# Optimization experiments

Hardware: AMD Instinct MI355X
Metric: run time of the kernel (lower is better)

The kernel has to match this reference:

```python
import jax, jax.numpy as jnp
import numpy as np

N_TRAIN = 131072
M_TEST = 65536
T_SPAN = 100.0
D = 3  # Matern-5/2 state dim


def setup_inputs() -> dict:
    key = jax.random.key(0)
    k1, k2, k3, k4 = jax.random.split(key, 4)
    times = jnp.sort(jax.random.uniform(k1, (N_TRAIN,), jnp.float32) * T_SPAN)
    t_star = jnp.sort(jax.random.uniform(k2, (M_TEST,), jnp.float32) * T_SPAN)
    # positive site precisions, site naturals scaled so pseudo-targets are O(1)
    site_nat2 = jax.random.uniform(k3, (N_TRAIN,), jnp.float32) * 4.0 + 0.5
    site_nat1 = jax.random.normal(k4, (N_TRAIN,), jnp.float32) * site_nat2
    return dict(
        times=times,
        t_star=t_star,
        site_nat1=site_nat1,
        site_nat2=site_nat2,
        variance=jnp.float32(1.0),
        lengthscale=jnp.float32(0.5),
        mean_const=jnp.float32(0.1),
    )


def _matern52_sde(variance, lengthscale):
    lam = jnp.sqrt(5.0).astype(jnp.float32) / lengthscale
    F = jnp.array([[0.0, 1.0, 0.0],
                   [0.0, 0.0, 1.0],
                   [0.0, 0.0, 0.0]], jnp.float32)
    F = F.at[2, 0].set(-lam ** 3).at[2, 1].set(-3.0 * lam ** 2).at[2, 2].set(-3.0 * lam)
    kappa = lam ** 2 / 3.0
    P_inf = variance * jnp.array([[1.0, 0.0, 0.0],
                                  [0.0, 0.0, 0.0],
                                  [0.0, 0.0, 0.0]], jnp.float32)
    P_inf = P_inf.at[0, 2].set(-variance * kappa)
    P_inf = P_inf.at[2, 0].set(-variance * kappa)
    P_inf = P_inf.at[1, 1].set(variance * kappa)
    P_inf = P_inf.at[2, 2].set(variance * lam ** 4)
    H = jnp.array([[1.0, 0.0, 0.0]], jnp.float32)
    return F, H, P_inf, lam


def _discretise(F, P_inf, lam, dt):
    # (F + lam I) is nilpotent of index 3 -> exact expm
    I = jnp.eye(D, dtype=jnp.float32)
    Nm = F + lam * I
    Nm2 = Nm @ Nm
    dt_ = dt[:, None, None]
    A = jnp.exp(-lam * dt)[:, None, None] * (I + dt_ * Nm + 0.5 * dt_ ** 2 * Nm2)
    APA = jnp.einsum('tij,jk,tlk->til', A, P_inf, A)
    Q = P_inf - APA
    return A, Q


def _kalman_filter(H, P_inf, A_seq, Q_seq, residual, is_obs, R_full):
    h = H[0]  # [D]

    def step(carry, inp):
        m, P = carry
        A, Q, r, obs, R = inp
        m_pred = A @ m
        P_pred = A @ P @ A.T + Q
        S = h @ P_pred @ h + R
        K = obs * (P_pred @ h) / S  # masked gain: test points skip update
        v = r - m_pred @ h
        m_f = m_pred + K * v
        P_f = P_pred - jnp.outer(K, K) * S
        return (m_f, P_f), (m_pred, P_pred, m_f, P_f)

    init = (jnp.zeros(D, jnp.float32), P_inf)
    _, (m_pred, P_pred, m_filt, P_filt) = jax.lax.scan(
        step, init, (A_seq, Q_seq, residual, is_obs, R_full))
    return m_pred, P_pred, m_filt, P_filt


def _rts_smoother(m_pred, P_pred, m_filt, P_filt, A_seq):
    def back(carry, inp):
        m_s_next, P_s_next = carry
        m_f, P_f, A_n, m_p_n, P_p_n = inp
        G = jnp.linalg.solve(P_p_n, A_n @ P_f).T  # P_f A^T P_pred^{-1}
        m_s = m_f + G @ (m_s_next - m_p_n)
        P_s = P_f + G @ (P_s_next - P_p_n) @ G.T
        return (m_s, P_s), (m_s, P_s)

    init = (m_filt[-1], P_filt[-1])
    xs = (m_filt[:-1], P_filt[:-1], A_seq[1:], m_pred[1:], P_pred[1:])
    _, (m_s, P_s) = jax.lax.scan(back, init, xs, reverse=True)
    m_smooth = jnp.concatenate([m_s, m_filt[-1:]], axis=0)
    P_smooth = jnp.concatenate([P_s, P_filt[-1:]], axis=0)
    return m_smooth, P_smooth


def reference(times, t_star, site_nat1, site_nat2, variance, lengthscale, mean_const):
    F, H, P_inf, lam = _matern52_sde(variance, lengthscale)
    N = times.shape[0]
    M = t_star.shape[0]
    merged = jnp.concatenate([times, t_star])
    order = jnp.argsort(merged)  # jnp.argsort is stable
    merged_sorted = merged[order]
    is_obs = jnp.concatenate([jnp.ones(N, jnp.float32), jnp.zeros(M, jnp.float32)])[order]
    pseudo_targets = site_nat1 / site_nat2
    residual_full = jnp.concatenate([pseudo_targets - mean_const,
                                     jnp.zeros(M, jnp.float32)])[order]
    R_full = jnp.concatenate([jnp.reciprocal(site_nat2), jnp.ones(M, jnp.float32)])[order]
    dt_full = jnp.concatenate([jnp.zeros(1, jnp.float32), jnp.diff(merged_sorted)])
    A_seq, Q_seq = _discretise(F, P_inf, lam, dt_full)
    m_pred, P_pred, m_filt, P_filt = _kalman_filter(
        H, P_inf, A_seq, Q_seq, residual_full, is_obs, R_full)
    m_smooth, P_smooth = _rts_smoother(m_pred, P_pred, m_filt, P_filt, A_seq)
    inv_order = jnp.argsort(order)
    test_positions = inv_order[N:]
    m_test = m_smooth[test_positions]
    P_test = P_smooth[test_positions]
    means = m_test @ H[0] + mean_const  # H = [1,0,0]
    vars_ = jnp.einsum('i,tij,j->t', H[0], P_test, H[0])
    return means, jnp.maximum(vars_, 0.0)
```

## Files before the change

kernel.cpp:

```cpp
#include <hip/hip_runtime.h>
#include <math.h>

#define DEV __device__ __forceinline__

constexpr int N_TRAIN = 131072;
constexpr int M_TEST  = 65536;
constexpr int T_TOT   = N_TRAIN + M_TEST;
constexpr int TPB     = 64;
constexpr int NBLK    = T_TOT / TPB;
constexpr int GRP     = 64;
constexpr int NGRP    = NBLK / GRP;
constexpr int FE_P    = 27;

DEV void mm(const float* X, const float* Y, float* Z) {
#pragma unroll
  for (int i = 0; i < 3; ++i)
#pragma unroll
    for (int j = 0; j < 3; ++j)
      Z[i*3+j] = X[i*3]*Y[j] + X[i*3+1]*Y[3+j] + X[i*3+2]*Y[6+j];
}
DEV void mmnt(const float* X, const float* Y, float* Z) {
#pragma unroll
  for (int i = 0; i < 3; ++i)
#pragma unroll
    for (int j = 0; j < 3; ++j)
      Z[i*3+j] = X[i*3]*Y[j*3] + X[i*3+1]*Y[j*3+1] + X[i*3+2]*Y[j*3+2];
}
DEV void mtn(const float* X, const float* Y, float* Z) {
#pragma unroll
  for (int i = 0; i < 3; ++i)
#pragma unroll
    for (int j = 0; j < 3; ++j)
      Z[i*3+j] = X[i]*Y[j] + X[3+i]*Y[3+j] + X[6+i]*Y[6+j];
}
DEV void mv(const float* X, const float* v, float* w) {
#pragma unroll
  for (int i = 0; i < 3; ++i) w[i] = X[i*3]*v[0] + X[i*3+1]*v[1] + X[i*3+2]*v[2];
}
DEV void mtv(const float* X, const float* v, float* w) {
#pragma unroll
  for (int i = 0; i < 3; ++i) w[i] = X[i]*v[0] + X[3+i]*v[1] + X[6+i]*v[2];
}
DEV void inv3f(const float* m, float* o) {
  float c00 = m[4]*m[8] - m[5]*m[7];
  float c10 = m[5]*m[6] - m[3]*m[8];
  float c20 = m[3]*m[7] - m[4]*m[6];
  float det = m[0]*c00 + m[1]*c10 + m[2]*c20;
  float id = 1.0f / det;
  o[0] = c00*id; o[1] = (m[2]*m[7]-m[1]*m[8])*id; o[2] = (m[1]*m[5]-m[2]*m[4])*id;
  o[3] = c10*id; o[4] = (m[0]*m[8]-m[2]*m[6])*id; o[5] = (m[2]*m[3]-m[0]*m[5])*id;
  o[6] = c20*id; o[7] = (m[1]*m[6]-m[0]*m[7])*id; o[8] = (m[0]*m[4]-m[1]*m[3])*id;
}
DEV void inv3d(const float* mf_, float* o) {
  double m0=mf_[0], m1=mf_[1], m2=mf_[2], m3=mf_[3], m4=mf_[4],
         m5=mf_[5], m6=mf_[6], m7=mf_[7], m8=mf_[8];
  double c00 = m4*m8 - m5*m7;
  double c10 = m5*m6 - m3*m8;
  double c20 = m3*m7 - m4*m6;
  double det = m0*c00 + m1*c10 + m2*c20;
  double id = 1.0 / det;
  o[0] = (float)(c00*id); o[1] = (float)((m2*m7-m1*m8)*id); o[2] = (float)((m1*m5-m2*m4)*id);
  o[3] = (float)(c10*id); o[4] = (float)((m0*m8-m2*m6)*id); o[5] = (float)((m2*m3-m0*m5)*id);
  o[6] = (float)(c20*id); o[7] = (float)((m1*m6-m0*m7)*id); o[8] = (float)((m0*m4-m1*m3)*id);
}
DEV void symm(float* P) {
  float a = 0.5f*(P[1]+P[3]), b = 0.5f*(P[2]+P[6]), c = 0.5f*(P[5]+P[7]);
  P[1]=P[3]=a; P[2]=P[6]=b; P[5]=P[7]=c;
}
DEV void st_state(const float* m, const float* P, float* g) {
  g[0]=m[0]; g[1]=m[1]; g[2]=m[2];
  g[3]=P[0]; g[4]=P[1]; g[5]=P[2]; g[6]=P[4]; g[7]=P[5]; g[8]=P[8];
}
DEV void ld_state(const float* g, float* m, float* P) {
  m[0]=g[0]; m[1]=g[1]; m[2]=g[2];
  P[0]=g[3]; P[1]=g[4]; P[2]=g[5];
  P[3]=g[4]; P[4]=g[6]; P[5]=g[7];
  P[6]=g[5]; P[7]=g[7]; P[8]=g[8];
}

struct Model { float lam, v, kap, l4; };
DEV Model make_model(const float* varp, const float* ellp) {
  Model M; M.v = varp[0];
  float ell = ellp[0];
  M.lam = sqrtf(5.0f) / ell;
  M.kap = M.lam * M.lam / 3.0f;
  float l2 = M.lam * M.lam;
  M.l4 = l2 * l2;
  return M;
}
DEV void pinf(const Model& M, float* P) {
  float vk = M.v * M.kap;
  P[0]=M.v; P[1]=0;  P[2]=-vk;
  P[3]=0;   P[4]=vk; P[5]=0;
  P[6]=-vk; P[7]=0;  P[8]=M.v*M.l4;
}
DEV void make_AQ(const Model& M, float dt, float* A, float* Q) {
  float lam = M.lam, l2 = lam*lam, l3 = l2*lam, l4 = M.l4;
  float e = __expf(-lam * dt);
  float h = 0.5f * dt * dt;
  A[0] = e*(1.0f + dt*lam + h*l2);
  A[1] = e*(dt + 2.0f*h*lam);
  A[2] = e*h;
  A[3] = e*(-h*l3);
  A[4] = e*(1.0f + dt*lam - 2.0f*h*l2);
  A[5] = e*(dt - h*lam);
  A[6] = e*(-dt*l3 + h*l4);
  A[7] = e*(-3.0f*dt*l2 + 2.0f*h*l3);
  A[8] = e*(1.0f - 2.0f*dt*lam + h*l2);
  float vk = M.v * M.kap, vl4 = M.v * M.l4;
  float B[9];
#pragma unroll
  for (int i = 0; i < 3; ++i) {
    B[i*3+0] =  A[i*3+0]*M.v - A[i*3+2]*vk;
    B[i*3+1] =  A[i*3+1]*vk;
    B[i*3+2] = -A[i*3+0]*vk  + A[i*3+2]*vl4;
  }
  float Pi[9]; pinf(M, Pi);
#pragma unroll
  for (int i = 0; i < 3; ++i)
#pragma unroll
    for (int j = 0; j < 3; ++j)
      Q[i*3+j] = Pi[i*3+j] - (B[i*3]*A[j*3] + B[i*3+1]*A[j*3+1] + B[i*3+2]*A[j*3+2]);
}

struct FE { float A[9]; float b[3]; float C[9]; float h[3]; float J[9]; };

DEV FE fe_identity() {
  FE e;
#pragma unroll
  for (int i=0;i<9;++i){ e.A[i]=0.0f; e.C[i]=0.0f; e.J[i]=0.0f; }
  e.A[0]=e.A[4]=e.A[8]=1.0f;
  e.b[0]=e.b[1]=e.b[2]=0.0f; e.h[0]=e.h[1]=e.h[2]=0.0f;
  return e;
}
DEV void fe_store27(const FE& e, float* g) {
#pragma unroll
  for (int i=0;i<9;++i) g[i]=e.A[i];
  g[9]=e.b[0]; g[10]=e.b[1]; g[11]=e.b[2];
  g[12]=e.C[0]; g[13]=e.C[1]; g[14]=e.C[2]; g[15]=e.C[4]; g[16]=e.C[5]; g[17]=e.C[8];
  g[18]=e.h[0]; g[19]=e.h[1]; g[20]=e.h[2];
  g[21]=e.J[0]; g[22]=e.J[1]; g[23]=e.J[2]; g[24]=e.J[4]; g[25]=e.J[5]; g[26]=e.J[8];
}
DEV FE fe_load27(const float* g) {
  FE e;
#pragma unroll
  for (int i=0;i<9;++i) e.A[i]=g[i];
  e.b[0]=g[9]; e.b[1]=g[10]; e.b[2]=g[11];
  e.C[0]=g[12]; e.C[1]=g[13]; e.C[2]=g[14]; e.C[3]=g[13]; e.C[4]=g[15];
  e.C[5]=g[16]; e.C[6]=g[14]; e.C[7]=g[16]; e.C[8]=g[17];
  e.h[0]=g[18]; e.h[1]=g[19]; e.h[2]=g[20];
  e.J[0]=g[21]; e.J[1]=g[22]; e.J[2]=g[23]; e.J[3]=g[22]; e.J[4]=g[24];
  e.J[5]=g[25]; e.J[6]=g[23]; e.J[7]=g[25]; e.J[8]=g[26];
  return e;
}
DEV void fe_storeT(const FE& e, float* g, int idx, int n) {
#pragma unroll
  for (int i=0;i<9;++i) g[i*n+idx]=e.A[i];
#pragma unroll
  for (int i=0;i<3;++i) g[(9+i)*n+idx]=e.b[i];
  g[12*n+idx]=e.C[0]; g[13*n+idx]=e.C[1]; g[14*n+idx]=e.C[2];
  g[15*n+idx]=e.C[4]; g[16*n+idx]=e.C[5]; g[17*n+idx]=e.C[8];
#pragma unroll
  for (int i=0;i<3;++i) g[(18+i)*n+idx]=e.h[i];
  g[21*n+idx]=e.J[0]; g[22*n+idx]=e.J[1]; g[23*n+idx]=e.J[2];
  g[24*n+idx]=e.J[4]; g[25*n+idx]=e.J[5]; g[26*n+idx]=e.J[8];
}
DEV FE fe_loadT(const float* g, int idx, int n) {
  FE e;
#pragma unroll
  for (int i=0;i<9;++i) e.A[i]=g[i*n+idx];
#pragma unroll
  for (int i=0;i<3;++i) e.b[i]=g[(9+i)*n+idx];
  float c0=g[12*n+idx], c1=g[13*n+idx], c2=g[14*n+idx],
        c4=g[15*n+idx], c5=g[16*n+idx], c8=g[17*n+idx];
  e.C[0]=c0; e.C[1]=c1; e.C[2]=c2; e.C[3]=c1; e.C[4]=c4; e.C[5]=c5;
  e.C[6]=c2; e.C[7]=c5; e.C[8]=c8;
#pragma unroll
  for (int i=0;i<3;++i) e.h[i]=g[(18+i)*n+idx];
  float j0=g[21*n+idx], j1=g[22*n+idx], j2=g[23*n+idx],
        j4=g[24*n+idx], j5=g[25*n+idx], j8=g[26*n+idx];
  e.J[0]=j0; e.J[1]=j1; e.J[2]=j2; e.J[3]=j1; e.J[4]=j4; e.J[5]=j5;
  e.J[6]=j2; e.J[7]=j5; e.J[8]=j8;
  return e;
}
DEV void fe_loadT_state(const float* g, int idx, int n, float* m, float* P) {
#pragma unroll
  for (int i=0;i<3;++i) m[i]=g[(9+i)*n+idx];
  float c0=g[12*n+idx], c1=g[13*n+idx], c2=g[14*n+idx],
        c4=g[15*n+idx], c5=g[16*n+idx], c8=g[17*n+idx];
  P[0]=c0; P[1]=c1; P[2]=c2; P[3]=c1; P[4]=c4; P[5]=c5; P[6]=c2; P[7]=c5; P[8]=c8;
}
DEV FE fe_shfl_up(const FE& e, int d) {
  FE o;
#pragma unroll
  for (int i=0;i<9;++i) o.A[i]=__shfl_up(e.A[i], d, 64);
#pragma unroll
  for (int i=0;i<3;++i) o.b[i]=__shfl_up(e.b[i], d, 64);
  float c0=__shfl_up(e.C[0],d,64), c1=__shfl_up(e.C[1],d,64), c2=__shfl_up(e.C[2],d,64),
        c4=__shfl_up(e.C[4],d,64), c5=__shfl_up(e.C[5],d,64), c8=__shfl_up(e.C[8],d,64);
  o.C[0]=c0; o.C[1]=c1; o.C[2]=c2; o.C[3]=c1; o.C[4]=c4; o.C[5]=c5;
  o.C[6]=c2; o.C[7]=c5; o.C[8]=c8;
#pragma unroll
  for (int i=0;i<3;++i) o.h[i]=__shfl_up(e.h[i], d, 64);
  float j0=__shfl_up(e.J[0],d,64), j1=__shfl_up(e.J[1],d,64), j2=__shfl_up(e.J[2],d,64),
        j4=__shfl_up(e.J[4],d,64), j5=__shfl_up(e.J[5],d,64), j8=__shfl_up(e.J[8],d,64);
  o.J[0]=j0; o.J[1]=j1; o.J[2]=j2; o.J[3]=j1; o.J[4]=j4; o.J[5]=j5;
  o.J[6]=j2; o.J[7]=j5; o.J[8]=j8;
  return o;
}
DEV FE build_felem(const Model& M, float dt, float obsf, float rf, float Rf_, bool first) {
  FE E;
  float r = rf, R = Rf_;
  float g = (obsf > 0.5f) ? 1.0f : 0.0f;
  if (first) {
#pragma unroll
    for (int i=0;i<9;++i){ E.A[i]=0.0f; E.J[i]=0.0f; }
    E.h[0]=E.h[1]=E.h[2]=0.0f;
    float Pi[9]; pinf(M, Pi);
    float S = Pi[0] + R;
    float f = g / S;
    float K0=Pi[0]*f, K1=Pi[3]*f, K2=Pi[6]*f;
    E.b[0]=K0*r; E.b[1]=K1*r; E.b[2]=K2*r;
    E.C[0]=Pi[0]-S*K0*K0; E.C[1]=Pi[1]-S*K0*K1; E.C[2]=Pi[2]-S*K0*K2;
    E.C[3]=Pi[3]-S*K1*K0; E.C[4]=Pi[4]-S*K1*K1; E.C[5]=Pi[5]-S*K1*K2;
    E.C[6]=Pi[6]-S*K2*K0; E.C[7]=Pi[7]-S*K2*K1; E.C[8]=Pi[8]-S*K2*K2;
    return E;
  }
  float Am[9], Q[9]; make_AQ(M, dt, Am, Q);
  float S = Q[0] + R, iS = g / S;
  float K0=Q[0]*iS, K1=Q[3]*iS, K2=Q[6]*iS;
#pragma unroll
  for (int j = 0; j < 3; ++j) {
    E.A[j]   = Am[j]   - K0*Am[j];
    E.A[3+j] = Am[3+j] - K1*Am[j];
    E.A[6+j] = Am[6+j] - K2*Am[j];
    E.C[j]   = Q[j]    - K0*Q[j];
    E.C[3+j] = Q[3+j]  - K1*Q[j];
    E.C[6+j] = Q[6+j]  - K2*Q[j];
  }
  E.b[0]=K0*r; E.b[1]=K1*r; E.b[2]=K2*r;
  float riS = r*iS;
  E.h[0]=Am[0]*riS; E.h[1]=Am[1]*riS; E.h[2]=Am[2]*riS;
#pragma unroll
  for (int i = 0; i < 3; ++i)
#pragma unroll
    for (int j = 0; j < 3; ++j)
      E.J[i*3+j] = Am[i]*Am[j]*iS;
  return E;
}
DEV FE fcompose(const FE& x, const FE& y) {
  const float *A1=x.A,*b1=x.b,*C1=x.C,*h1=x.h,*J1=x.J;
  const float *A2=y.A,*b2=y.b,*C2=y.C,*h2=y.h,*J2=y.J;
  FE o;
  float Mx[9]; mm(C1,J2,Mx); Mx[0]+=1.0f; Mx[4]+=1.0f; Mx[8]+=1.0f;
  float Mi[9]; inv3f(Mx,Mi);
  float T1[9]; mm(A2,Mi,T1);
  mm(T1,A1,o.A);
  float u[3]; mv(C1,h2,u); u[0]+=b1[0]; u[1]+=b1[1]; u[2]+=b1[2];
  mv(T1,u,o.b); o.b[0]+=b2[0]; o.b[1]+=b2[1]; o.b[2]+=b2[2];
  float t2[9]; mm(T1,C1,t2);
  mmnt(t2,A2,o.C);
#pragma unroll
  for (int i=0;i<9;++i) o.C[i]+=C2[i];
  float tmp[9]; mm(Mi,A1,tmp);
  float w[3]; mv(J2,b1,w);
  w[0]=h2[0]-w[0]; w[1]=h2[1]-w[1]; w[2]=h2[2]-w[2];
  mtv(tmp,w,o.h); o.h[0]+=h1[0]; o.h[1]+=h1[1]; o.h[2]+=h1[2];
  float V[9]; mm(J2,A1,V);
  mtn(tmp,V,o.J);
#pragma unroll
  for (int i=0;i<9;++i) o.J[i]+=J1[i];
  symm(o.C); symm(o.J);
  return o;
}
DEV void fapply(const FE& y, float* m, float* P) {
  float Mx[9]; mm(P, y.J, Mx); Mx[0]+=1.0f; Mx[4]+=1.0f; Mx[8]+=1.0f;
  float Mi[9]; inv3f(Mx, Mi);
  float T1[9]; mm(y.A, Mi, T1);
  float u[3]; mv(P, y.h, u); u[0]+=m[0]; u[1]+=m[1]; u[2]+=m[2];
  float mn[3]; mv(T1, u, mn);
  m[0]=mn[0]+y.b[0]; m[1]=mn[1]+y.b[1]; m[2]=mn[2]+y.b[2];
  float t2[9]; mm(T1, P, t2);
  float Pn[9]; mmnt(t2, y.A, Pn);
#pragma unroll
  for (int i=0;i<9;++i) P[i]=Pn[i]+y.C[i];
  symm(P);
}
DEV void fstep(const Model& M, float dt, float obsf, float rf, float Rf_,
               float* m, float* P) {
  float A[9], Q[9]; make_AQ(M, dt, A, Q);
  float mp[3]; mv(A, m, mp);
  float W[9]; mmnt(P, A, W);
  float Pp[9]; mm(A, W, Pp);
#pragma unroll
  for (int i=0;i<9;++i) Pp[i]+=Q[i];
  float S = Pp[0] + Rf_;
  float f = (obsf > 0.5f) ? (1.0f/S) : 0.0f;
  float K0=Pp[0]*f, K1=Pp[3]*f, K2=Pp[6]*f;
  float v = rf - mp[0];
  m[0]=mp[0]+K0*v; m[1]=mp[1]+K1*v; m[2]=mp[2]+K2*v;
  P[0]=Pp[0]-S*K0*K0; P[1]=Pp[1]-S*K0*K1; P[2]=Pp[2]-S*K0*K2;
  P[3]=Pp[3]-S*K1*K0; P[4]=Pp[4]-S*K1*K1; P[5]=Pp[5]-S*K1*K2;
  P[6]=Pp[6]-S*K2*K0; P[7]=Pp[7]-S*K2*K1; P[8]=Pp[8]-S*K2*K2;
  symm(P);
}

struct SE { float G[9]; float c[3]; float U[9]; };

DEV SE se_identity() {
  SE s;
#pragma unroll
  for (int i=0;i<9;++i){ s.G[i]=0.0f; s.U[i]=0.0f; }
  s.G[0]=s.G[4]=s.G[8]=1.0f;
  s.c[0]=s.c[1]=s.c[2]=0.0f;
  return s;
}
DEV void se_store(const SE& s, float* g) {
#pragma unroll
  for (int i=0;i<9;++i) g[i]=s.G[i];
  g[9]=s.c[0]; g[10]=s.c[1]; g[11]=s.c[2];
  g[12]=s.U[0]; g[13]=s.U[1]; g[14]=s.U[2]; g[15]=s.U[4]; g[16]=s.U[5]; g[17]=s.U[8];
}
DEV SE se_load(const float* g) {
  SE s;
#pragma unroll
  for (int i=0;i<9;++i) s.G[i]=g[i];
  s.c[0]=g[9]; s.c[1]=g[10]; s.c[2]=g[11];
  s.U[0]=g[12]; s.U[1]=g[13]; s.U[2]=g[14];
  s.U[3]=g[13]; s.U[4]=g[15]; s.U[5]=g[16];
  s.U[6]=g[14]; s.U[7]=g[16]; s.U[8]=g[17];
  return s;
}
DEV void se_storeT(const SE& s, float* g, int idx, int n) {
#pragma unroll
  for (int i=0;i<9;++i) g[i*n+idx]=s.G[i];
#pragma unroll
  for (int i=0;i<3;++i) g[(9+i)*n+idx]=s.c[i];
  g[12*n+idx]=s.U[0]; g[13*n+idx]=s.U[1]; g[14*n+idx]=s.U[2];
  g[15*n+idx]=s.U[4]; g[16*n+idx]=s.U[5]; g[17*n+idx]=s.U[8];
}
DEV SE se_loadT(const float* g, int idx, int n) {
  SE s;
#pragma unroll
  for (int i=0;i<9;++i) s.G[i]=g[i*n+idx];
#pragma unroll
  for (int i=0;i<3;++i) s.c[i]=g[(9+i)*n+idx];
  float u0=g[12*n+idx], u1=g[13*n+idx], u2=g[14*n+idx],
        u4=g[15*n+idx], u5=g[16*n+idx], u8=g[17*n+idx];
  s.U[0]=u0; s.U[1]=u1; s.U[2]=u2;
  s.U[3]=u1; s.U[4]=u4; s.U[5]=u5;
  s.U[6]=u2; s.U[7]=u5; s.U[8]=u8;
  return s;
}
DEV SE se_shfl_down(const SE& s, int d) {
  SE o;
#pragma unroll
  for (int i=0;i<9;++i) o.G[i]=__shfl_down(s.G[i], d, 64);
#pragma unroll
  for (int i=0;i<3;++i) o.c[i]=__shfl_down(s.c[i], d, 64);
  float u0=__shfl_down(s.U[0],d,64), u1=__shfl_down(s.U[1],d,64), u2=__shfl_down(s.U[2],d,64),
        u4=__shfl_down(s.U[4],d,64), u5=__shfl_down(s.U[5],d,64), u8=__shfl_down(s.U[8],d,64);
  o.U[0]=u0; o.U[1]=u1; o.U[2]=u2; o.U[3]=u1; o.U[4]=u4; o.U[5]=u5;
  o.U[6]=u2; o.U[7]=u5; o.U[8]=u8;
  return o;
}
DEV SE scompose(const SE& x, const SE& y) {
  SE o;
  mm(x.G, y.G, o.G);
  float t[3]; mv(x.G, y.c, t);
  o.c[0]=t[0]+x.c[0]; o.c[1]=t[1]+x.c[1]; o.c[2]=t[2]+x.c[2];
  float T[9]; mm(x.G, y.U, T);
  mmnt(T, x.G, o.U);
#pragma unroll
  for (int i=0;i<9;++i) o.U[i]+=x.U[i];
  symm(o.U);
  return o;
}
DEV void sapply(const SE& s, float* m, float* P) {
  float t[3]; mv(s.G, m, t);
  float T[9]; mm(s.G, P, T);
  float Pn[9]; mmnt(T, s.G, Pn);
  m[0]=t[0]+s.c[0]; m[1]=t[1]+s.c[1]; m[2]=t[2]+s.c[2];
#pragma unroll
  for (int i=0;i<9;++i) P[i]=Pn[i]+s.U[i];
  symm(P);
}
DEV SE selem_from_state(const Model& M, const float* m, const float* P, float dtn) {
  SE s;
  float A[9], Q[9]; make_AQ(M, dtn, A, Q);
  float W[9]; mmnt(P, A, W);
  float Pp[9]; mm(A, W, Pp);
#pragma unroll
  for (int j=0;j<9;++j) Pp[j]+=Q[j];
  float Pi_[9]; inv3d(Pp, Pi_);
  mm(W, Pi_, s.G);
  float mp[3]; mv(A, m, mp);
  float gm[3]; mv(s.G, mp, gm);
  s.c[0]=m[0]-gm[0]; s.c[1]=m[1]-gm[1]; s.c[2]=m[2]-gm[2];
  float GW[9]; mmnt(s.G, W, GW);
#pragma unroll
  for (int j=0;j<9;++j) s.U[j]=P[j]-GW[j];
  symm(s.U);
  return s;
}

__global__ void k_merge(const float* __restrict__ times, const float* __restrict__ tstar,
                        const float* __restrict__ n1, const float* __restrict__ n2,
                        const float* __restrict__ mcp,
                        float4* pk, int* oix) {
  int g = blockIdx.x*blockDim.x + threadIdx.x;
  if (g >= T_TOT) return;
  float mc = mcp[0];
  if (g < N_TRAIN) {
    int i = g;
    float t = times[i];
    int lo = 0, hi = M_TEST;
    while (lo < hi) { int mid=(lo+hi)>>1; if (tstar[mid] < t) lo=mid+1; else hi=mid; }
    int p = i + lo;
    float s2 = n2[i];
    pk[p] = make_float4(t, n1[i]/s2 - mc, 1.0f/s2, 1.0f);
    oix[p] = -1;
  } else {
    int j = g - N_TRAIN;
    float t = tstar[j];
    int lo = 0, hi = N_TRAIN;
    while (lo < hi) { int mid=(lo+hi)>>1; if (times[mid] <= t) lo=mid+1; else hi=mid; }
    int p = j + lo;
    pk[p] = make_float4(t, 0.f, 1.f, 0.f);
    oix[p] = j;
  }
}

__global__ __launch_bounds__(TPB) void k_f1(
    const float* varp, const float* ellp, const float4* __restrict__ pk,
    float* tIncl, float* blkAgg) {
  int l = threadIdx.x, b = blockIdx.x;
  int t = b*TPB + l;
  Model M = make_model(varp, ellp);
  float4 q = pk[t];
  float dt = (t == 0) ? 0.0f : (q.x - pk[t-1].x);
  FE run = build_felem(M, dt, q.w, q.y, q.z, t == 0);
  for (int d = 1; d < TPB; d <<= 1) {
    FE oth = fe_shfl_up(run, d);
    FE comp = fcompose(oth, run);
    if (l >= d) run = comp;
  }
  fe_storeT(run, tIncl, t, T_TOT);
  if (l == TPB-1) fe_storeT(run, blkAgg, b, NBLK);
}

__global__ __launch_bounds__(TPB) void k_f2a(const float* __restrict__ blkAgg,
                                             float* blkIncl2, float* grpAgg) {
  int l = threadIdx.x, gb = blockIdx.x;
  int b = gb*GRP + l;
  FE run = fe_loadT(blkAgg, b, NBLK);
  for (int d = 1; d < TPB; d <<= 1) {
    FE oth = fe_shfl_up(run, d);
    FE comp = fcompose(oth, run);
    if (l >= d) run = comp;
  }
  fe_storeT(run, blkIncl2, b, NBLK);
  if (l == GRP-1) fe_store27(run, grpAgg + gb*FE_P);
}

__global__ __launch_bounds__(TPB) void k_f2b(const float* __restrict__ grpAgg,
                                             float* grpPref) {
  int j = threadIdx.x;
  FE run = (j < NGRP) ? fe_load27(grpAgg + j*FE_P) : fe_identity();
  for (int d = 1; d < TPB; d <<= 1) {
    FE oth = fe_shfl_up(run, d);
    FE comp = fcompose(oth, run);
    if (j >= d) run = comp;
  }
  FE X = fe_shfl_up(run, 1);
  if (j < NGRP) {
    if (j == 0) X = fe_identity();
    fe_store27(X, grpPref + j*FE_P);
  }
}

__global__ __launch_bounds__(TPB) void k_f3(
    const float* varp, const float* ellp, const float4* __restrict__ pk,
    const float* __restrict__ tIncl, const float* __restrict__ blkIncl2,
    const float* __restrict__ grpPref,
    float* out5, float* blkAggS, float* xT) {
  int l = threadIdx.x, b = blockIdx.x;
  int t = b*TPB + l;
  int g = b >> 6, lb = b & (GRP-1);
  Model M = make_model(varp, ellp);
  float m[3], P[9];
  if (t == 0) {
    m[0]=m[1]=m[2]=0.0f; pinf(M, P);
  } else if (g == 0 && lb == 0) {
    fe_loadT_state(tIncl, t-1, T_TOT, m, P);
  } else if (g == 0) {
    fe_loadT_state(blkIncl2, b-1, NBLK, m, P);
    if (l > 0) { FE y = fe_loadT(tIncl, t-1, T_TOT); fapply(y, m, P); }
  } else {
    const float* gp = grpPref + g*FE_P;
    m[0]=gp[9]; m[1]=gp[10]; m[2]=gp[11];
    P[0]=gp[12]; P[1]=gp[13]; P[2]=gp[14];
    P[3]=gp[13]; P[4]=gp[15]; P[5]=gp[16];
    P[6]=gp[14]; P[7]=gp[16]; P[8]=gp[17];
    if (lb > 0) { FE y = fe_loadT(blkIncl2, b-1, NBLK); fapply(y, m, P); }
    if (l  > 0) { FE y = fe_loadT(tIncl,  t-1, T_TOT); fapply(y, m, P); }
  }
  float4 q = pk[t];
  float dt = (t == 0) ? 0.0f : (q.x - pk[t-1].x);
  fstep(M, dt, q.w, q.y, q.z, m, P);
  SE e;
  if (t < T_TOT-1) {
    float dtn = pk[t+1].x - q.x;
    e = selem_from_state(M, m, P, dtn);
  } else {
    e = se_identity();
    xT[0]=m[0]; xT[1]=m[1]; xT[2]=m[2];
    xT[3]=P[0]; xT[4]=P[1]; xT[5]=P[2];
    xT[6]=P[4]; xT[7]=P[5]; xT[8]=P[8];
  }
  SE Macc = e;
  for (int d = 1; d < TPB; d <<= 1) {
    SE oth = se_shfl_down(Macc, d);
    SE c = scompose(Macc, oth);
    if (l + d < TPB) Macc = c;
  }
  out5[0*T_TOT+t] = Macc.G[0];
  out5[1*T_TOT+t] = Macc.G[1];
  out5[2*T_TOT+t] = Macc.G[2];
  out5[3*T_TOT+t] = Macc.c[0];
  out5[4*T_TOT+t] = Macc.U[0];
  if (l == 0) se_storeT(Macc, blkAggS, b, NBLK);
}

__global__ __launch_bounds__(TPB) void k_s2a(const float* __restrict__ blkAggS,
                                             float* blkSuf2, float* grpAggS) {
  int l = threadIdx.x, gb = blockIdx.x;
  int b = gb*GRP + l;
  SE run = se_loadT(blkAggS, b, NBLK);
  for (int d = 1; d < TPB; d <<= 1) {
    SE oth = se_shfl_down(run, d);
    SE comp = scompose(run, oth);
    if (l + d < TPB) run = comp;
  }
  se_storeT(run, blkSuf2, b, NBLK);
  if (l == 0) se_store(run, grpAggS + gb*18);
}

__global__ __launch_bounds__(TPB) void k_s2b(const float* __restrict__ grpAggS,
                                             const float* __restrict__ xT,
                                             float* gExit) {
  int j = threadIdx.x;
  SE run = (j < NGRP) ? se_load(grpAggS + j*18) : se_identity();
  for (int d = 1; d < TPB; d <<= 1) {
    SE oth = se_shfl_down(run, d);
    SE comp = scompose(run, oth);
    if (j + d < TPB) run = comp;
  }
  SE Sx = se_shfl_down(run, 1);
  if (j < NGRP) {
    float m[3] = { xT[0], xT[1], xT[2] };
    float P[9] = { xT[3],xT[4],xT[5], xT[4],xT[6],xT[7], xT[5],xT[7],xT[8] };
    if (j < NGRP-1) sapply(Sx, m, P);
    st_state(m, P, gExit + j*9);
  }
}

__global__ __launch_bounds__(256) void k_s3(
    const float* mcp, const float* __restrict__ out5,
    const float* __restrict__ blkSuf2, const float* __restrict__ gExit,
    const int* __restrict__ oix, float* out) {
  int t = blockIdx.x*256 + threadIdx.x;
  int b = t >> 6;
  int g = b >> 6, lb = b & (GRP-1);
  float mc = mcp[0];
  float m[3], P[9];
  ld_state(gExit + g*9, m, P);
  if (lb < GRP-1) {
    SE s = se_loadT(blkSuf2, b+1, NBLK);
    sapply(s, m, P);
  }
  float g0 = out5[0*T_TOT+t], g1 = out5[1*T_TOT+t], g2 = out5[2*T_TOT+t];
  float c0 = out5[3*T_TOT+t], u00 = out5[4*T_TOT+t];
  float mm0 = g0*m[0] + g1*m[1] + g2*m[2] + c0;
  float q0 = g0*P[0] + g1*P[3] + g2*P[6];
  float q1 = g0*P[1] + g1*P[4] + g2*P[7];
  float q2 = g0*P[2] + g1*P[5] + g2*P[8];
  float v00 = q0*g0 + q1*g1 + q2*g2 + u00;
  int j = oix[t];
  if (j >= 0) { out[j] = mm0 + mc; out[M_TEST + j] = fmaxf(v00, 0.0f); }
}

extern "C" void kernel_launch(void* const* d_in, const int* in_sizes, int n_in,
                              void* d_out, int out_size, void* d_ws, size_t ws_size,
                              hipStream_t stream) {
  const float* times = (const float*)d_in[0];
  const float* tstar = (const float*)d_in[1];
  const float* n1    = (const float*)d_in[2];
  const float* n2    = (const float*)d_in[3];
  const float* varp  = (const float*)d_in[4];
  const float* ellp  = (const float*)d_in[5];
  const float* mcp   = (const float*)d_in[6];
  float* out = (float*)d_out;

  size_t off = 0;
  auto take = [&](size_t bytes) {
    char* p = (char*)d_ws + off;
    off += (bytes + 255) & ~(size_t)255;
    return (void*)p;
  };
  float4* pk     = (float4*)take(sizeof(float4) * T_TOT);
  int*    oix    = (int*)   take(sizeof(int)    * T_TOT);
  float*  tIncl  = (float*) take(sizeof(float)  * FE_P * T_TOT);
  float*  blkAgg = (float*) take(sizeof(float)  * FE_P * NBLK);
  float*  blkIncl2=(float*) take(sizeof(float)  * FE_P * NBLK);
  float*  grpAgg = (float*) take(sizeof(float)  * FE_P * NGRP);
  float*  grpPref= (float*) take(sizeof(float)  * FE_P * NGRP);
  float*  out5   = (float*) take(sizeof(float)  * 5  * T_TOT);
  float*  blkAggS= (float*) take(sizeof(float)  * 18 * NBLK);
  float*  blkSuf2= (float*) take(sizeof(float)  * 18 * NBLK);
  float*  grpAggS= (float*) take(sizeof(float)  * 18 * NGRP);
  float*  gExit  = (float*) take(sizeof(float)  * 9  * NGRP);
  float*  xT     = (float*) take(sizeof(float)  * 9);
  (void)ws_size; (void)in_sizes; (void)n_in; (void)out_size;

  k_merge<<<(T_TOT+255)/256, 256, 0, stream>>>(times, tstar, n1, n2, mcp, pk, oix);
  k_f1   <<<NBLK, TPB, 0, stream>>>(varp, ellp, pk, tIncl, blkAgg);
  k_f2a  <<<NGRP, TPB, 0, stream>>>(blkAgg, blkIncl2, grpAgg);
  k_f2b  <<<1, TPB, 0, stream>>>(grpAgg, grpPref);
  k_f3   <<<NBLK, TPB, 0, stream>>>(varp, ellp, pk, tIncl, blkIncl2, grpPref, out5, blkAggS, xT);
  k_s2a  <<<NGRP, TPB, 0, stream>>>(blkAggS, blkSuf2, grpAggS);
  k_s2b  <<<1, TPB, 0, stream>>>(grpAggS, xT, gExit);
  k_s3   <<<T_TOT/256, 256, 0, stream>>>(mcp, out5, blkSuf2, gExit, oix, out);
}
```

Baseline: 142.3 us.

## Recompute intra-block filter scan instead of storing it; fold top-level scans into consumers

The forward pass no longer writes the per-element inclusive scan (27 floats per element) to global memory. k_f3 instead rebuilds the filter elements and redoes the in-wave scan, using the exclusive result directly. The small single-block group-level scans (k_f2b, k_s2b) are removed: every block of k_f3 and k_s3 redundantly scans the 48 group aggregates itself. This drops two kernel launches and a large global write/read round trip, at the cost of repeating scan arithmetic in every block.

```diff
diff --git a/kernel.cpp b/kernel.cpp
--- a/kernel.cpp
+++ b/kernel.cpp
@@ -182,13 +182,6 @@
   e.J[0]=j0; e.J[1]=j1; e.J[2]=j2; e.J[3]=j1; e.J[4]=j4; e.J[5]=j5;
   e.J[6]=j2; e.J[7]=j5; e.J[8]=j8;
   return e;
-}
-DEV void fe_loadT_state(const float* g, int idx, int n, float* m, float* P) {
-#pragma unroll
-  for (int i=0;i<3;++i) m[i]=g[(9+i)*n+idx];
-  float c0=g[12*n+idx], c1=g[13*n+idx], c2=g[14*n+idx],
-        c4=g[15*n+idx], c5=g[16*n+idx], c8=g[17*n+idx];
-  P[0]=c0; P[1]=c1; P[2]=c2; P[3]=c1; P[4]=c4; P[5]=c5; P[6]=c2; P[7]=c5; P[8]=c8;
 }
 DEV FE fe_shfl_up(const FE& e, int d) {
   FE o;
@@ -433,7 +426,7 @@
 
 __global__ __launch_bounds__(TPB) void k_f1(
     const float* varp, const float* ellp, const float4* __restrict__ pk,
-    float* tIncl, float* blkAgg) {
+    float* blkAgg) {
   int l = threadIdx.x, b = blockIdx.x;
   int t = b*TPB + l;
   Model M = make_model(varp, ellp);
@@ -445,7 +438,6 @@
     FE comp = fcompose(oth, run);
     if (l >= d) run = comp;
   }
-  fe_storeT(run, tIncl, t, T_TOT);
   if (l == TPB-1) fe_storeT(run, blkAgg, b, NBLK);
 }
 
@@ -463,50 +455,46 @@
   if (l == GRP-1) fe_store27(run, grpAgg + gb*FE_P);
 }
 
-__global__ __launch_bounds__(TPB) void k_f2b(const float* __restrict__ grpAgg,
-                                             float* grpPref) {
-  int j = threadIdx.x;
-  FE run = (j < NGRP) ? fe_load27(grpAgg + j*FE_P) : fe_identity();
-  for (int d = 1; d < TPB; d <<= 1) {
-    FE oth = fe_shfl_up(run, d);
-    FE comp = fcompose(oth, run);
-    if (j >= d) run = comp;
-  }
-  FE X = fe_shfl_up(run, 1);
-  if (j < NGRP) {
-    if (j == 0) X = fe_identity();
-    fe_store27(X, grpPref + j*FE_P);
-  }
-}
-
 __global__ __launch_bounds__(TPB) void k_f3(
     const float* varp, const float* ellp, const float4* __restrict__ pk,
-    const float* __restrict__ tIncl, const float* __restrict__ blkIncl2,
-    const float* __restrict__ grpPref,
+    const float* __restrict__ blkIncl2, const float* __restrict__ grpAgg,
     float* out5, float* blkAggS, float* xT) {
   int l = threadIdx.x, b = blockIdx.x;
   int t = b*TPB + l;
   int g = b >> 6, lb = b & (GRP-1);
   Model M = make_model(varp, ellp);
-  float m[3], P[9];
-  if (t == 0) {
-    m[0]=m[1]=m[2]=0.0f; pinf(M, P);
-  } else if (g == 0 && lb == 0) {
-    fe_loadT_state(tIncl, t-1, T_TOT, m, P);
-  } else if (g == 0) {
-    fe_loadT_state(blkIncl2, b-1, NBLK, m, P);
-    if (l > 0) { FE y = fe_loadT(tIncl, t-1, T_TOT); fapply(y, m, P); }
-  } else {
-    const float* gp = grpPref + g*FE_P;
-    m[0]=gp[9]; m[1]=gp[10]; m[2]=gp[11];
-    P[0]=gp[12]; P[1]=gp[13]; P[2]=gp[14];
-    P[3]=gp[13]; P[4]=gp[15]; P[5]=gp[16];
-    P[6]=gp[14]; P[7]=gp[16]; P[8]=gp[17];
-    if (lb > 0) { FE y = fe_loadT(blkIncl2, b-1, NBLK); fapply(y, m, P); }
-    if (l  > 0) { FE y = fe_loadT(tIncl,  t-1, T_TOT); fapply(y, m, P); }
-  }
   float4 q = pk[t];
   float dt = (t == 0) ? 0.0f : (q.x - pk[t-1].x);
+  FE ex;
+  {
+    FE run = build_felem(M, dt, q.w, q.y, q.z, t == 0);
+    for (int d = 1; d < TPB; d <<= 1) {
+      FE oth = fe_shfl_up(run, d);
+      FE comp = fcompose(oth, run);
+      if (l >= d) run = comp;
+    }
+    ex = fe_shfl_up(run, 1);
+  }
+  float m[3], P[9];
+  {
+    FE run = (l < NGRP) ? fe_load27(grpAgg + l*FE_P) : fe_identity();
+    for (int d = 1; d < 64; d <<= 1) {
+      FE oth = fe_shfl_up(run, d);
+      FE comp = fcompose(oth, run);
+      if (l >= d) run = comp;
+    }
+    if (g == 0) {
+      m[0]=m[1]=m[2]=0.0f; pinf(M, P);
+    } else {
+      int src = g-1;
+      m[0]=__shfl(run.b[0],src,64); m[1]=__shfl(run.b[1],src,64); m[2]=__shfl(run.b[2],src,64);
+      float c0=__shfl(run.C[0],src,64), c1=__shfl(run.C[1],src,64), c2=__shfl(run.C[2],src,64),
+            c4=__shfl(run.C[4],src,64), c5=__shfl(run.C[5],src,64), c8=__shfl(run.C[8],src,64);
+      P[0]=c0; P[1]=c1; P[2]=c2; P[3]=c1; P[4]=c4; P[5]=c5; P[6]=c2; P[7]=c5; P[8]=c8;
+    }
+  }
+  if (lb > 0) { FE y = fe_loadT(blkIncl2, b-1, NBLK); fapply(y, m, P); }
+  if (l  > 0) { fapply(ex, m, P); }
   fstep(M, dt, q.w, q.y, q.z, m, P);
   SE e;
   if (t < T_TOT-1) {
@@ -546,35 +534,36 @@
   if (l == 0) se_store(run, grpAggS + gb*18);
 }
 
-__global__ __launch_bounds__(TPB) void k_s2b(const float* __restrict__ grpAggS,
-                                             const float* __restrict__ xT,
-                                             float* gExit) {
-  int j = threadIdx.x;
-  SE run = (j < NGRP) ? se_load(grpAggS + j*18) : se_identity();
-  for (int d = 1; d < TPB; d <<= 1) {
-    SE oth = se_shfl_down(run, d);
-    SE comp = scompose(run, oth);
-    if (j + d < TPB) run = comp;
-  }
-  SE Sx = se_shfl_down(run, 1);
-  if (j < NGRP) {
-    float m[3] = { xT[0], xT[1], xT[2] };
-    float P[9] = { xT[3],xT[4],xT[5], xT[4],xT[6],xT[7], xT[5],xT[7],xT[8] };
-    if (j < NGRP-1) sapply(Sx, m, P);
-    st_state(m, P, gExit + j*9);
-  }
-}
-
 __global__ __launch_bounds__(256) void k_s3(
     const float* mcp, const float* __restrict__ out5,
-    const float* __restrict__ blkSuf2, const float* __restrict__ gExit,
+    const float* __restrict__ blkSuf2, const float* __restrict__ grpAggS,
+    const float* __restrict__ xT,
     const int* __restrict__ oix, float* out) {
-  int t = blockIdx.x*256 + threadIdx.x;
+  __shared__ float sSt[9];
+  int tid = threadIdx.x;
+  int t = blockIdx.x*256 + tid;
   int b = t >> 6;
   int g = b >> 6, lb = b & (GRP-1);
+  if (tid < 64) {
+    int j = tid;
+    SE run = (j < NGRP) ? se_load(grpAggS + j*18) : se_identity();
+    for (int d = 1; d < 64; d <<= 1) {
+      SE oth = se_shfl_down(run, d);
+      SE comp = scompose(run, oth);
+      if (j + d < 64) run = comp;
+    }
+    SE Sx = se_shfl_down(run, 1);
+    if (j == g) {
+      float m[3] = { xT[0], xT[1], xT[2] };
+      float P[9] = { xT[3],xT[4],xT[5], xT[4],xT[6],xT[7], xT[5],xT[7],xT[8] };
+      if (g < NGRP-1) sapply(Sx, m, P);
+      st_state(m, P, sSt);
+    }
+  }
+  __syncthreads();
   float mc = mcp[0];
   float m[3], P[9];
-  ld_state(gExit + g*9, m, P);
+  ld_state(sSt, m, P);
   if (lb < GRP-1) {
     SE s = se_loadT(blkSuf2, b+1, NBLK);
     sapply(s, m, P);
@@ -608,27 +597,22 @@
     off += (bytes + 255) & ~(size_t)255;
     return (void*)p;
   };
-  float4* pk     = (float4*)take(sizeof(float4) * T_TOT);
-  int*    oix    = (int*)   take(sizeof(int)    * T_TOT);
-  float*  tIncl  = (float*) take(sizeof(float)  * FE_P * T_TOT);
-  float*  blkAgg = (float*) take(sizeof(float)  * FE_P * NBLK);
-  float*  blkIncl2=(float*) take(sizeof(float)  * FE_P * NBLK);
-  float*  grpAgg = (float*) take(sizeof(float)  * FE_P * NGRP);
-  float*  grpPref= (float*) take(sizeof(float)  * FE_P * NGRP);
-  float*  out5   = (float*) take(sizeof(float)  * 5  * T_TOT);
-  float*  blkAggS= (float*) take(sizeof(float)  * 18 * NBLK);
-  float*  blkSuf2= (float*) take(sizeof(float)  * 18 * NBLK);
-  float*  grpAggS= (float*) take(sizeof(float)  * 18 * NGRP);
-  float*  gExit  = (float*) take(sizeof(float)  * 9  * NGRP);
-  float*  xT     = (float*) take(sizeof(float)  * 9);
+  float4* pk      = (float4*)take(sizeof(float4) * T_TOT);
+  int*    oix     = (int*)   take(sizeof(int)    * T_TOT);
+  float*  blkAgg  = (float*) take(sizeof(float)  * FE_P * NBLK);
+  float*  blkIncl2= (float*) take(sizeof(float)  * FE_P * NBLK);
+  float*  grpAgg  = (float*) take(sizeof(float)  * FE_P * NGRP);
+  float*  out5    = (float*) take(sizeof(float)  * 5  * T_TOT);
+  float*  blkAggS = (float*) take(sizeof(float)  * 18 * NBLK);
+  float*  blkSuf2 = (float*) take(sizeof(float)  * 18 * NBLK);
+  float*  grpAggS = (float*) take(sizeof(float)  * 18 * NGRP);
+  float*  xT      = (float*) take(sizeof(float)  * 16);
   (void)ws_size; (void)in_sizes; (void)n_in; (void)out_size;
 
   k_merge<<<(T_TOT+255)/256, 256, 0, stream>>>(times, tstar, n1, n2, mcp, pk, oix);
-  k_f1   <<<NBLK, TPB, 0, stream>>>(varp, ellp, pk, tIncl, blkAgg);
+  k_f1   <<<NBLK, TPB, 0, stream>>>(varp, ellp, pk, blkAgg);
   k_f2a  <<<NGRP, TPB, 0, stream>>>(blkAgg, blkIncl2, grpAgg);
-  k_f2b  <<<1, TPB, 0, stream>>>(grpAgg, grpPref);
-  k_f3   <<<NBLK, TPB, 0, stream>>>(varp, ellp, pk, tIncl, blkIncl2, grpPref, out5, blkAggS, xT);
+  k_f3   <<<NBLK, TPB, 0, stream>>>(varp, ellp, pk, blkIncl2, grpAgg, out5, blkAggS, xT);
   k_s2a  <<<NGRP, TPB, 0, stream>>>(blkAggS, blkSuf2, grpAggS);
-  k_s2b  <<<1, TPB, 0, stream>>>(grpAggS, xT, gExit);
-  k_s3   <<<T_TOT/256, 256, 0, stream>>>(mcp, out5, blkSuf2, gExit, oix, out);
-}
+  k_s3   <<<T_TOT/256, 256, 0, stream>>>(mcp, out5, blkSuf2, grpAggS, xT, oix, out);
+}
```

Result: slower. 151.6 us (+6.5%).
